# Optimization experiments

Hardware: AMD Instinct MI355X
Metric: run time of the kernel (lower is better)

## Reference

```python
import jax, jax.numpy as jnp
import numpy as np
from jax import lax

ORDER = 6
WN = 0.5 / 50.0          # highpass_cutoff / (orig_fs/2)
UP, DOWN = 16, 25        # 64/100 reduced by gcd 4 (scipy resample_poly)
HALF_LEN = 10 * DOWN     # scipy kaiser half length = 10*max_rate
NTAPS = 2 * HALF_LEN + 1
PADLEN = 21              # sosfiltfilt default: 3*(2*n_sections+1), 3 biquads
CHANNELS = np.array([126, 125, 48, 112, 67, 93, 10, 61, 39, 108])
D_MODEL = 16
LN_EPS = 1e-5


def _butter_hp_sos(order, wn):
    # scipy.signal.butter(order, wn, btype='high', output='sos') in pure numpy
    fs = 2.0
    warped = 2.0 * fs * np.tan(np.pi * wn / fs)
    m = np.arange(-order + 1, order, 2)
    p = -np.exp(1j * np.pi * m / (2 * order))     # analog LP prototype poles
    k = np.real(1.0 / np.prod(-p))                # lp2hp gain (no zeros)
    p = warped / p                                # lp2hp poles; zeros at s=0
    z = np.zeros(order)
    fs2 = 2.0 * fs                                # bilinear, fs=2
    k = k * np.real(np.prod(fs2 - z) / np.prod(fs2 - p))
    z = (fs2 + z) / (fs2 - z)                     # digital zeros, all +1
    p = (fs2 + p) / (fs2 - p)
    pp = p[np.imag(p) > 0]
    pp = pp[np.argsort(-np.abs(np.abs(pp) - 1.0))]  # closest to unit circle last
    sos = []
    for i, pi in enumerate(pp):
        b = np.array([1.0, -2.0, 1.0]) * (k if i == 0 else 1.0)
        a = np.array([1.0, -2.0 * pi.real, np.abs(pi) ** 2])
        sos.append(np.concatenate([b, a]))
    return np.array(sos)


def _sosfilt_zi(sos):
    # scipy.signal.sosfilt_zi: steady-state of step response per section
    n = sos.shape[0]
    zi = np.zeros((n, 2))
    scale = 1.0
    for s in range(n):
        b0, b1, b2, _, a1, a2 = sos[s]
        A = np.array([[1.0 + a1, -1.0], [a2, 1.0]])
        B = np.array([b1 - a1 * b0, b2 - a2 * b0])
        zi[s] = scale * np.linalg.solve(A, B)
        scale *= (b0 + b1 + b2) / (1.0 + a1 + a2)
    return zi


SOS = _butter_hp_sos(ORDER, WN)
ZI = _sosfilt_zi(SOS)


def _resample_fir():
    # scipy firwin(2*half_len+1, 1/max_rate, window=('kaiser',5.0)) * up
    fc = 1.0 / DOWN
    m = np.arange(NTAPS) - (NTAPS - 1) / 2.0
    h = fc * np.sinc(fc * m) * np.kaiser(NTAPS, 5.0)
    h /= h.sum()
    return h * UP


H_BASE = _resample_fir()


def _pos_encoding(max_len, d):
    pos = np.arange(max_len)[:, None].astype(np.float64)
    div = np.exp(np.arange(0, d, 2) * (-np.log(10000.0) / d))
    pe = np.zeros((max_len, d))
    pe[:, 0::2] = np.sin(pos * div)
    pe[:, 1::2] = np.cos(pos * div)
    return pe.astype(np.float32)


PE = _pos_encoding(3840, D_MODEL)


def _sosfilt(x, zi):
    # x: (N,T), zi: (N,3,2). Cascade of biquads, transposed direct form II.
    sos = jnp.asarray(SOS, x.dtype)
    nsec = SOS.shape[0]

    def step(z, xt):
        v = xt
        zs = []
        for s in range(nsec):  # fixed tiny cascade, unrolled inside scan
            b0, b1, b2, a1, a2 = sos[s, 0], sos[s, 1], sos[s, 2], sos[s, 4], sos[s, 5]
            y = b0 * v + z[s][0]
            zs.append((b1 * v - a1 * y + z[s][1], b2 * v - a2 * y))
            v = y
        return tuple(zs), v

    z0 = tuple((zi[:, s, 0], zi[:, s, 1]) for s in range(nsec))
    _, y = lax.scan(step, z0, x.T)
    return y.T


def _sosfiltfilt(x):
    # scipy.signal.sosfiltfilt with default odd padding, padlen=21
    zi = jnp.asarray(ZI, x.dtype)
    front = 2.0 * x[:, :1] - x[:, PADLEN:0:-1]
    back = 2.0 * x[:, -1:] - x[:, -2:-PADLEN - 2:-1]
    ext = jnp.concatenate([front, x, back], axis=1)
    y = _sosfilt(ext, zi[None] * ext[:, 0, None, None])
    y = y[:, ::-1]
    y = _sosfilt(y, zi[None] * y[:, 0, None, None])
    return y[:, ::-1][:, PADLEN:-PADLEN]


def _resample_poly(x):
    # scipy.signal.resample_poly(x, 64, 100): upfirdn via dilated conv
    T = x.shape[-1]
    n_out = (T * UP) // DOWN + int((T * UP) % DOWN != 0)
    n_pre_pad = DOWN - HALF_LEN % DOWN
    n_pre_remove = (HALF_LEN + n_pre_pad) // DOWN

    def outlen(lh):
        return (((T - 1) * UP + lh) - 1) // DOWN + 1

    n_post = 0
    while outlen(NTAPS + n_pre_pad + n_post) < n_out + n_pre_remove:
        n_post += 1
    h = np.concatenate([np.zeros(n_pre_pad), H_BASE, np.zeros(n_post)])
    L = h.size
    rhs = jnp.asarray(h[::-1].copy(), x.dtype).reshape(1, 1, L)
    y = lax.conv_general_dilated(x[:, None, :], rhs, window_strides=(DOWN,),
                                 padding=[(L - 1, L - 1)], lhs_dilation=(UP,),
                                 dimension_numbers=('NCH', 'OIH', 'NCH'))
    return y[:, 0, n_pre_remove:n_pre_remove + n_out]


def _ln(x, g, b):
    mu = x.mean(-1, keepdims=True)
    var = ((x - mu) ** 2).mean(-1, keepdims=True)
    return (x - mu) * lax.rsqrt(var + LN_EPS) * g + b


def setup_inputs() -> dict:
    key = jax.random.key(0)
    ks = jax.random.split(key, 20)
    f32 = jnp.float32
    d = {
        'x': jax.random.normal(ks[0], (64, 128, 2000), f32),
        'conv_w': jax.random.normal(ks[1], (16, 10, 3), f32) * 0.15,
        'conv_b': jnp.zeros((16,), f32),
        'ln0_g': jnp.ones((16,), f32), 'ln0_b': jnp.zeros((16,), f32),
        'wqkv': jax.random.normal(ks[2], (48, 16), f32) * 0.125,
        'bqkv': jnp.zeros((48,), f32),
        'wo': jax.random.normal(ks[3], (16, 16), f32) * 0.25,
        'bo': jnp.zeros((16,), f32),
        'w1': jax.random.normal(ks[4], (32, 16), f32) * 0.2,
        'b1': jnp.zeros((32,), f32),
        'w2': jax.random.normal(ks[5], (16, 32), f32) * 0.2,
        'b2': jnp.zeros((16,), f32),
        'ln1_g': jnp.ones((16,), f32), 'ln1_b': jnp.zeros((16,), f32),
        'ln2_g': jnp.ones((16,), f32), 'ln2_b': jnp.zeros((16,), f32),
        'wfc': jax.random.normal(ks[6], (1, 16), f32) * 0.3,
        'bfc': jnp.zeros((1,), f32),
    }
    return d


def reference(x, conv_w, conv_b, ln0_g, ln0_b, wqkv, bqkv, wo, bo,
              w1, b1, w2, b2, ln1_g, ln1_b, ln2_g, ln2_b, wfc, bfc):
    B = x.shape[0]
    # remove Cz (last channel) then gather interesting channels
    x = x[:, :-1, :][:, jnp.asarray(CHANNELS), :]        # (B,10,T)
    x = x - x.mean(axis=1, keepdims=True)                # CAR
    C, T = x.shape[1], x.shape[2]
    xf = _sosfiltfilt(x.reshape(B * C, T))               # zero-phase highpass
    xr = _resample_poly(xf)                              # 100 Hz -> 64 Hz
    x = xr.reshape(B, C, -1)
    x = jnp.tanh(x)                                      # artifact_scale = 1.0
    mean = x.mean(axis=2, keepdims=True)                 # zscore, unbiased std
    var = ((x - mean) ** 2).sum(axis=2, keepdims=True) / (x.shape[2] - 1)
    std = jnp.maximum(jnp.sqrt(var), 1e-6)
    x = (x - mean) / std
    # conv1d k=3 pad=1 (10 -> 16) + relu
    x = lax.conv_general_dilated(x, conv_w, (1,), [(1, 1)],
                                 dimension_numbers=('NCH', 'OIH', 'NCH'))
    x = jax.nn.relu(x + conv_b[None, :, None])
    x = x.transpose(0, 2, 1)                             # (B,S,16)
    x = _ln(x, ln0_g, ln0_b)
    x = x + jnp.asarray(PE[:x.shape[1]], x.dtype)[None]
    # TransformerEncoderLayer, post-norm, nhead=1, relu FFN (eval: no dropout)
    qkv = x @ wqkv.T + bqkv
    q, k, v = jnp.split(qkv, 3, axis=-1)
    att = jax.nn.softmax(jnp.einsum('bqd,bkd->bqk', q, k) * 0.25, axis=-1)
    a = jnp.einsum('bqk,bkd->bqd', att, v) @ wo.T + bo
    x = _ln(x + a, ln1_g, ln1_b)
    f = jax.nn.relu(x @ w1.T + b1) @ w2.T + b2
    x = _ln(x + f, ln2_g, ln2_b)
    pooled = x.mean(axis=1)                              # adaptive avg pool -> 1
    return pooled @ wfc.T + bfc                          # (B,1)
```

## Files before the change

### kernel.cpp

```cpp
#include <hip/hip_runtime.h>
#include <cmath>
#include <complex>
#include <algorithm>

#ifndef M_PI
#define M_PI 3.14159265358979323846
#endif

typedef _Float16 f16x8 __attribute__((ext_vector_type(8)));
typedef _Float16 f16x4 __attribute__((ext_vector_type(4)));
typedef float f32x4 __attribute__((ext_vector_type(4)));

struct FiltArg {
  double b0[3], b1[3], b2[3], a1[3], a2[3];
  double zi0[3], zi1[3];
};
struct CorArg { double CA[16 * 6]; };
struct EigArg {
  double Pm[36], Pinv[36];
  double czi[6];
  double lam_re[3], lam_im[3];
  double lami_re[3], lami_im[3];
};
struct FirArg { float h[526]; };

static void design_sos(FiltArg& sa) {
  const int order = 6;
  const double wn = 0.5 / 50.0;
  const double fs = 2.0;
  double warped = 2.0 * fs * std::tan(M_PI * wn / fs);
  std::complex<double> p[6];
  for (int i = 0; i < order; i++) {
    int m = -order + 1 + 2 * i;
    p[i] = -std::exp(std::complex<double>(0.0, M_PI * m / (2.0 * order)));
  }
  std::complex<double> prod1(1, 0);
  for (int i = 0; i < 6; i++) prod1 *= -p[i];
  double k = (1.0 / prod1).real();
  for (int i = 0; i < 6; i++) p[i] = warped / p[i];
  const double fs2 = 2.0 * fs;
  std::complex<double> num(1, 0), den(1, 0);
  for (int i = 0; i < 6; i++) { num *= fs2; den *= (fs2 - p[i]); }
  k *= (num / den).real();
  for (int i = 0; i < 6; i++) p[i] = (fs2 + p[i]) / (fs2 - p[i]);
  std::complex<double> pp[3]; int n = 0;
  for (int i = 0; i < 6; i++) if (p[i].imag() > 0) pp[n++] = p[i];
  std::stable_sort(pp, pp + 3,
    [](const std::complex<double>& A, const std::complex<double>& B) {
      return std::fabs(std::abs(A) - 1.0) > std::fabs(std::abs(B) - 1.0);
    });
  double sos[3][6];
  for (int s = 0; s < 3; s++) {
    double g = (s == 0) ? k : 1.0;
    sos[s][0] = g; sos[s][1] = -2.0 * g; sos[s][2] = g;
    sos[s][3] = 1.0; sos[s][4] = -2.0 * pp[s].real(); sos[s][5] = std::norm(pp[s]);
  }
  double scale = 1.0;
  for (int s = 0; s < 3; s++) {
    double b0 = sos[s][0], b1 = sos[s][1], b2 = sos[s][2];
    double a1 = sos[s][4], a2 = sos[s][5];
    double det = 1.0 + a1 + a2;
    double r0 = b1 - a1 * b0, r1 = b2 - a2 * b0;
    double z0 = (r0 + r1) / det;
    double z1 = ((1.0 + a1) * r1 - a2 * r0) / det;
    sa.b0[s] = b0; sa.b1[s] = b1; sa.b2[s] = b2; sa.a1[s] = a1; sa.a2[s] = a2;
    sa.zi0[s] = scale * z0; sa.zi1[s] = scale * z1;
    scale *= (b0 + b1 + b2) / (1.0 + a1 + a2);
  }
}

static double host_step(const FiltArg& c, double z[6], double v) {
  for (int s = 0; s < 3; s++) {
    double y = c.b0[s] * v + z[2 * s];
    z[2 * s]     = c.b1[s] * v - c.a1[s] * y + z[2 * s + 1];
    z[2 * s + 1] = c.b2[s] * v - c.a2[s] * y;
    v = y;
  }
  return v;
}

static void build_filt(FiltArg& c, CorArg& co) {
  design_sos(c);
  for (int j = 0; j < 6; j++) {
    double z[6] = {0, 0, 0, 0, 0, 0};
    z[j] = 1.0;
    for (int i = 0; i < 16; i++) co.CA[i * 6 + j] = host_step(c, z, 0.0);
  }
}

static void build_eig(const FiltArg& c, EigArg& e) {
  double Pr[36];
  for (int s = 0; s < 3; s++) {
    double a1 = c.a1[s], a2 = c.a2[s];
    std::complex<double> disc = std::sqrt(std::complex<double>(a1 * a1 - 4.0 * a2, 0.0));
    std::complex<double> p = (-a1 + disc) / 2.0;
    if (p.imag() < 0) p = std::conj(p);
    std::complex<double> v[6] = {0, 0, 0, 0, 0, 0};
    v[2 * s] = 1.0;
    v[2 * s + 1] = a1 + p;
    std::complex<double> y = 1.0;
    for (int j = s + 1; j < 3; j++) {
      double b0j = c.b0[j], b1j = c.b1[j], b2j = c.b2[j];
      double a1j = c.a1[j], a2j = c.a2[j];
      std::complex<double> det = p * p + a1j * p + a2j;
      std::complex<double> r0 = (b1j - a1j * b0j) * y;
      std::complex<double> r1 = (b2j - a2j * b0j) * y;
      std::complex<double> z0 = (p * r0 + r1) / det;
      std::complex<double> z1 = ((p + a1j) * r1 - a2j * r0) / det;
      v[2 * j] = z0; v[2 * j + 1] = z1;
      y = b0j * y + z0;
    }
    for (int i = 0; i < 6; i++) {
      Pr[i * 6 + 2 * s]     = v[i].real();
      Pr[i * 6 + 2 * s + 1] = v[i].imag();
    }
    std::complex<double> lam = std::pow(p, 16);
    e.lam_re[s] = lam.real(); e.lam_im[s] = lam.imag();
    std::complex<double> li = 1.0 / lam;
    e.lami_re[s] = li.real(); e.lami_im[s] = li.imag();
  }
  for (int i = 0; i < 36; i++) e.Pm[i] = Pr[i];
  double M[6][12];
  for (int i = 0; i < 6; i++)
    for (int j = 0; j < 6; j++) { M[i][j] = Pr[i * 6 + j]; M[i][6 + j] = (i == j) ? 1.0 : 0.0; }
  for (int col = 0; col < 6; col++) {
    int piv = col;
    for (int i = col + 1; i < 6; i++)
      if (std::fabs(M[i][col]) > std::fabs(M[piv][col])) piv = i;
    if (piv != col) for (int j = 0; j < 12; j++) std::swap(M[col][j], M[piv][j]);
    double d = M[col][col];
    for (int j = 0; j < 12; j++) M[col][j] /= d;
    for (int i = 0; i < 6; i++) if (i != col) {
      double f = M[i][col];
      for (int j = 0; j < 12; j++) M[i][j] -= f * M[col][j];
    }
  }
  for (int i = 0; i < 6; i++)
    for (int j = 0; j < 6; j++) e.Pinv[i * 6 + j] = M[i][6 + j];
  double zv[6];
  for (int s = 0; s < 3; s++) { zv[2 * s] = c.zi0[s]; zv[2 * s + 1] = c.zi1[s]; }
  for (int i = 0; i < 6; i++) {
    double sum = 0.0;
    for (int j = 0; j < 6; j++) sum += e.Pinv[i * 6 + j] * zv[j];
    e.czi[i] = sum;
  }
}

static double bessel_i0(double x) {
  double s = 1.0, t = 1.0;
  for (int k = 1; k < 64; k++) {
    double u = x / (2.0 * k);
    t *= u * u; s += t;
    if (t < 1e-18 * s) break;
  }
  return s;
}

static void design_fir(FirArg& fa) {
  double h[501];
  const double fc = 1.0 / 25.0;
  double denom = bessel_i0(5.0);
  double sum = 0.0;
  for (int nn = 0; nn < 501; nn++) {
    double m = nn - 250.0;
    double xx = fc * m;
    double snc = (nn == 250) ? 1.0 : std::sin(M_PI * xx) / (M_PI * xx);
    double r = (2.0 * nn) / 500.0 - 1.0;
    double w = bessel_i0(5.0 * std::sqrt(std::max(0.0, 1.0 - r * r))) / denom;
    h[nn] = fc * snc * w; sum += h[nn];
  }
  for (int nn = 0; nn < 25; nn++) fa.h[nn] = 0.0f;
  for (int nn = 0; nn < 501; nn++) fa.h[25 + nn] = (float)(h[nn] / sum * 16.0);
}

__device__ inline double waveReduceSum(double v) {
  #pragma unroll
  for (int off = 32; off > 0; off >>= 1) v += __shfl_down(v, off, 64);
  return v;
}

__device__ inline void cpow_int(double br, double bi, int n, double& rr_, double& ri_) {
  double rr = 1.0, ri = 0.0;
  while (n) {
    if (n & 1) { double t = rr * br - ri * bi; ri = rr * bi + ri * br; rr = t; }
    double t2 = br * br - bi * bi; bi = 2.0 * br * bi; br = t2;
    n >>= 1;
  }
  rr_ = rr; ri_ = ri;
}

__global__ __launch_bounds__(256) void k_chansel_pe(const float* __restrict__ x,
                                                    float* __restrict__ xs,
                                                    float* __restrict__ pe,
                                                    float* __restrict__ out) {
  int gid = blockIdx.x;
  if (gid < 500) {
    int idx = gid * 256 + threadIdx.x;
    int b = idx / 2000, t = idx % 2000;
    const int ch[10] = {126, 125, 48, 112, 67, 93, 10, 61, 39, 108};
    const float* xb = x + (size_t)b * 128 * 2000;
    float v[10]; float s = 0.f;
    #pragma unroll
    for (int c = 0; c < 10; c++) { v[c] = xb[ch[c] * 2000 + t]; s += v[c]; }
    s *= 0.1f;
    #pragma unroll
    for (int c = 0; c < 10; c++) xs[((size_t)b * 10 + c) * 2000 + t] = v[c] - s;
  } else {
    int i = (gid - 500) * 256 + threadIdx.x;
    int t = i >> 4, d = i & 15, j = d >> 1;
    double div = exp(-((double)(2 * j)) * 0.5756462732485114);
    double a = (double)t * div;
    pe[i] = (float)((d & 1) ? cos(a) : sin(a));
    if (gid == 579 && threadIdx.x < 64) out[threadIdx.x] = 0.f;
  }
}

#define XR(t) xr[(t) + ((t) >> 5)]
#define YF(t) yf[(t) + ((t) >> 5)]
__global__ __launch_bounds__(128) void k_filtfilt(float* __restrict__ xs,
                                                  FiltArg c, CorArg co, EigArg eg) {
  __shared__ float xr[2112];
  __shared__ double yf[2112];
  __shared__ double wsum[3][2];
  int r = blockIdx.x;
  int gk = threadIdx.x;
  int lane = gk & 63;
  int wv = gk >> 6;
  float* x = xs + (size_t)r * 2000;

  float x0f = x[0], xlf = x[1999];
  for (int t = gk; t < 2048; t += 128) {
    float v;
    if (t < 21)        v = 2.f * x0f - x[21 - t];
    else if (t < 2021) v = x[t - 21];
    else if (t < 2042) v = 2.f * xlf - x[4019 - t];
    else               v = 0.f;
    XR(t) = v;
  }
  __syncthreads();

  double b0[3], b1[3], b2[3], a1[3], a2[3];
  #pragma unroll
  for (int s = 0; s < 3; s++) {
    b0[s] = c.b0[s]; b1[s] = c.b1[s]; b2[s] = c.b2[s];
    a1[s] = c.a1[s]; a2[s] = c.a2[s];
  }
  auto step = [&](double* z, double v) -> double {
    #pragma unroll
    for (int s = 0; s < 3; s++) {
      double y = b0[s] * v + z[2 * s];
      z[2 * s]     = b1[s] * v - a1[s] * y + z[2 * s + 1];
      z[2 * s + 1] = b2[s] * v - a2[s] * y;
      v = y;
    }
    return v;
  };

  auto eigscan = [&](double seed, const double* F, double* zst) {
    double G[6];
    #pragma unroll
    for (int i = 0; i < 6; i++) {
      double s = 0.0;
      #pragma unroll
      for (int j = 0; j < 6; j++) s += eg.Pinv[i * 6 + j] * F[j];
      G[i] = s;
    }
    double tre[3], tim[3], sre[3], sim[3];
    #pragma unroll
    for (int s3 = 0; s3 < 3; s3++) {
      double gre = G[2 * s3], gim = -G[2 * s3 + 1];
      double mre, mim;
      cpow_int(eg.lami_re[s3], eg.lami_im[s3], gk, mre, mim);
      tre[s3] = mre * gre - mim * gim;
      tim[s3] = mre * gim + mim * gre;
      double pr = tre[s3], pi = tim[s3];
      #pragma unroll
      for (int off = 1; off < 64; off <<= 1) {
        double ore = __shfl_up(pr, off, 64);
        double oim = __shfl_up(pi, off, 64);
        pr += (lane >= off) ? ore : 0.0;
        pi += (lane >= off) ? oim : 0.0;
      }
      sre[s3] = pr; sim[s3] = pi;
      if (wv == 0 && lane == 63) { wsum[s3][0] = pr; wsum[s3][1] = pi; }
    }
    __syncthreads();
    double coord[6];
    #pragma unroll
    for (int s3 = 0; s3 < 3; s3++) {
      double inc_re = sre[s3] + (wv ? wsum[s3][0] : 0.0);
      double inc_im = sim[s3] + (wv ? wsum[s3][1] : 0.0);
      double Sre = inc_re - tre[s3], Sim = inc_im - tim[s3];
      double c0re = seed * eg.czi[2 * s3];
      double c0im = -seed * eg.czi[2 * s3 + 1];
      double lkre, lkim;
      cpow_int(eg.lam_re[s3], eg.lam_im[s3], gk, lkre, lkim);
      double lm1re = lkre * eg.lami_re[s3] - lkim * eg.lami_im[s3];
      double lm1im = lkre * eg.lami_im[s3] + lkim * eg.lami_re[s3];
      if (gk == 0) { lm1re = 0.0; lm1im = 0.0; }
      double cre = lkre * c0re - lkim * c0im + lm1re * Sre - lm1im * Sim;
      double cim = lkre * c0im + lkim * c0re + lm1re * Sim + lm1im * Sre;
      coord[2 * s3] = cre;
      coord[2 * s3 + 1] = -cim;
    }
    #pragma unroll
    for (int i = 0; i < 6; i++) {
      double s = 0.0;
      #pragma unroll
      for (int j = 0; j < 6; j++) s += eg.Pm[i * 6 + j] * coord[j];
      zst[i] = s;
    }
  };

  int t0 = gk * 16;
  double z[6], yreg[16], zst[6];

  #pragma unroll
  for (int i = 0; i < 6; i++) z[i] = 0.0;
  for (int i = 0; i < 16; i++) yreg[i] = step(z, (double)XR(t0 + i));
  eigscan((double)XR(0), z, zst);
  for (int i = 0; i < 16; i++) {
    double corr = 0.0;
    #pragma unroll
    for (int j = 0; j < 6; j++) corr += co.CA[i * 6 + j] * zst[j];
    YF(t0 + i) = yreg[i] + corr;
  }
  __syncthreads();

  auto rin = [&](int j) -> double { return (j <= 2041) ? YF(2041 - j) : 0.0; };
  double seedB = YF(2041);
  #pragma unroll
  for (int i = 0; i < 6; i++) z[i] = 0.0;
  for (int i = 0; i < 16; i++) yreg[i] = step(z, rin(t0 + i));
  eigscan(seedB, z, zst);
  for (int i = 0; i < 16; i++) {
    int j = t0 + i;
    if (j >= 21 && j <= 2020) {
      double corr = 0.0;
      #pragma unroll
      for (int jj = 0; jj < 6; jj++) corr += co.CA[i * 6 + jj] * zst[jj];
      x[2020 - j] = (float)(yreg[i] + corr);
    }
  }
}

__global__ __launch_bounds__(256) void k_resample_norm(const float* __restrict__ xf,
                                                       float* __restrict__ xn,
                                                       FirArg fa) {
  __shared__ float xl[2000];
  __shared__ float hl[526];
  int r = blockIdx.x;
  const float* x = xf + (size_t)r * 2000;
  for (int i = threadIdx.x; i < 2000; i += 256) xl[i] = x[i];
  for (int i = threadIdx.x; i < 526; i += 256) hl[i] = fa.h[i];
  __syncthreads();
  float vals[5];
  #pragma unroll
  for (int kk = 0; kk < 5; kk++) {
    int o = threadIdx.x + kk * 256;
    int P = 25 * (o + 11);
    int phase = P & 15;
    float acc = 0.f;
    for (int m = phase; m <= 525; m += 16) {
      int idx = (P - m) >> 4;
      if (idx >= 0 && idx < 2000) acc += hl[m] * xl[idx];
    }
    vals[kk] = tanhf(acc);
  }
  double s = 0.0, ss = 0.0;
  #pragma unroll
  for (int kk = 0; kk < 5; kk++) {
    s += (double)vals[kk]; ss += (double)vals[kk] * (double)vals[kk];
  }
  s = waveReduceSum(s); ss = waveReduceSum(ss);
  __shared__ double red[8];
  int wid = threadIdx.x >> 6, lane = threadIdx.x & 63;
  if (lane == 0) { red[wid] = s; red[4 + wid] = ss; }
  __syncthreads();
  double S = red[0] + red[1] + red[2] + red[3];
  double SS = red[4] + red[5] + red[6] + red[7];
  double mean = S / 1280.0;
  double var = (SS - 1280.0 * mean * mean) / 1279.0;
  double sd = fmax(sqrt(fmax(var, 0.0)), 1e-6);
  float fmean = (float)mean, finv = (float)(1.0 / sd);
  #pragma unroll
  for (int kk = 0; kk < 5; kk++)
    xn[(size_t)r * 1280 + threadIdx.x + kk * 256] = (vals[kk] - fmean) * finv;
}

__global__ __launch_bounds__(256) void k_conv_ln_pe_qkv(const float* __restrict__ xn,
    const float* __restrict__ cw, const float* __restrict__ cb,
    const float* __restrict__ g0, const float* __restrict__ bt0,
    const float* __restrict__ wqkv, const float* __restrict__ bqkv,
    const float* __restrict__ pe,
    float* __restrict__ x0, float* __restrict__ Q,
    _Float16* __restrict__ Kp, _Float16* __restrict__ Vt_g) {
  __shared__ float w[480], bias[16], gg[16], gb[16];
  __shared__ float wq[768], bq[48];
  for (int i = threadIdx.x; i < 480; i += 256) w[i] = cw[i];
  for (int i = threadIdx.x; i < 768; i += 256) wq[i] = wqkv[i];
  if (threadIdx.x < 16) {
    bias[threadIdx.x] = cb[threadIdx.x];
    gg[threadIdx.x] = g0[threadIdx.x];
    gb[threadIdx.x] = bt0[threadIdx.x];
  }
  if (threadIdx.x < 48) bq[threadIdx.x] = bqkv[threadIdx.x];
  __syncthreads();
  int idx = blockIdx.x * 256 + threadIdx.x;
  int b = idx / 1280, t = idx % 1280;
  const float* xb = xn + (size_t)b * 10 * 1280;
  float in[10][3];
  #pragma unroll
  for (int i = 0; i < 10; i++)
    #pragma unroll
    for (int k = 0; k < 3; k++) {
      int tt = t - 1 + k;
      in[i][k] = (tt >= 0 && tt < 1280) ? xb[i * 1280 + tt] : 0.f;
    }
  float o[16];
  #pragma unroll
  for (int oc = 0; oc < 16; oc++) {
    float a = bias[oc];
    #pragma unroll
    for (int i = 0; i < 10; i++)
      #pragma unroll
      for (int k = 0; k < 3; k++) a += in[i][k] * w[oc * 30 + i * 3 + k];
    o[oc] = fmaxf(a, 0.f);
  }
  float mu = 0.f;
  #pragma unroll
  for (int d = 0; d < 16; d++) mu += o[d];
  mu *= (1.f / 16.f);
  float var = 0.f;
  #pragma unroll
  for (int d = 0; d < 16; d++) { float dd = o[d] - mu; var += dd * dd; }
  var *= (1.f / 16.f);
  float inv = 1.f / sqrtf(var + 1e-5f);
  float xv[16];
  float* outp = x0 + (size_t)idx * 16;
  const float* pep = pe + t * 16;
  #pragma unroll
  for (int d = 0; d < 16; d++) {
    xv[d] = (o[d] - mu) * inv * gg[d] + gb[d] + pep[d];
    outp[d] = xv[d];
  }
  float* qp = Q + (size_t)idx * 16;
  #pragma unroll
  for (int j = 0; j < 16; j++) {
    float a = bq[j];
    #pragma unroll
    for (int d = 0; d < 16; d++) a += xv[d] * wq[j * 16 + d];
    qp[j] = a;
  }
  {
    _Float16* kp = Kp + (size_t)idx * 32;
    #pragma unroll
    for (int j = 0; j < 16; j++) {
      float a = bq[16 + j];
      #pragma unroll
      for (int d = 0; d < 16; d++) a += xv[d] * wq[(16 + j) * 16 + d];
      kp[j] = (_Float16)a;
    }
    f16x8 zz;
    #pragma unroll
    for (int j = 0; j < 8; j++) zz[j] = (_Float16)0.f;
    *(f16x8*)&kp[16] = zz;
    *(f16x8*)&kp[24] = zz;
  }
  {
    _Float16* vt = Vt_g + (size_t)b * 16 * 1280 + t;
    #pragma unroll
    for (int j = 0; j < 16; j++) {
      float a = bq[32 + j];
      #pragma unroll
      for (int d = 0; d < 16; d++) a += xv[d] * wq[(32 + j) * 16 + d];
      vt[j * 1280] = (_Float16)a;
    }
  }
}

#define ATT_SHIFT 12.0f
__global__ __launch_bounds__(256) void k_attn_mfma(const float* __restrict__ Q,
    const _Float16* __restrict__ Kp, const _Float16* __restrict__ Vt_g,
    float* __restrict__ A) {
  __shared__ __align__(16) _Float16 Ks2[64 * 32];
  __shared__ __align__(16) _Float16 Vt[16 * 72];
  __shared__ __align__(16) _Float16 Pld[4][16 * 40];
  int tid = threadIdx.x;
  int b  = blockIdx.x / 20;
  int rg = blockIdx.x % 20;
  int wv = tid >> 6;
  int lane = tid & 63;
  int col = lane & 15;
  int quad = lane >> 4;
  size_t base = (size_t)b * 1280;
  int row0 = rg * 64 + wv * 16;

  f16x8 qf;
  #pragma unroll
  for (int j = 0; j < 8; j++) qf[j] = (_Float16)0.f;
  if (quad < 2) {
    const float* qp = Q + (base + row0 + col) * 16 + quad * 8;
    #pragma unroll
    for (int j = 0; j < 8; j++) qf[j] = (_Float16)(0.25f * qp[j]);
  }
  f32x4 oacc = {0.f, 0.f, 0.f, 0.f};
  float lacc = 0.f;

  const _Float16* vt_b = Vt_g + (size_t)b * 16 * 1280;

  for (int s = 0; s < 20; s++) {
    __syncthreads();
    *(f16x8*)&Ks2[tid * 8] =
        *(const f16x8*)(Kp + (base + s * 64) * 32 + tid * 8);
    if (tid < 128) {
      int d = tid >> 3, qc = tid & 7;
      *(f16x8*)&Vt[d * 72 + qc * 8] =
          *(const f16x8*)(vt_b + d * 1280 + s * 64 + qc * 8);
    }
    __syncthreads();
    #pragma unroll
    for (int c = 0; c < 2; c++) {
      #pragma unroll
      for (int t = 0; t < 2; t++) {
        int keyoff = c * 32 + t * 16;
        f16x8 af = *(f16x8*)&Ks2[(keyoff + col) * 32 + quad * 8];
        f32x4 sf = {0.f, 0.f, 0.f, 0.f};
        sf = __builtin_amdgcn_mfma_f32_16x16x32_f16(af, qf, sf, 0, 0, 0);
        f16x4 ph;
        float psum = 0.f;
        #pragma unroll
        for (int r = 0; r < 4; r++) {
          float p = __expf(sf[r] - ATT_SHIFT);
          psum += p;
          ph[r] = (_Float16)p;
        }
        lacc += psum;
        *(f16x4*)&Pld[wv][col * 40 + t * 16 + quad * 4] = ph;
      }
      __syncthreads();
      f16x8 pf = *(f16x8*)&Pld[wv][col * 40 + quad * 8];
      f16x8 vf = *(f16x8*)&Vt[col * 72 + c * 32 + quad * 8];
      oacc = __builtin_amdgcn_mfma_f32_16x16x32_f16(pf, vf, oacc, 0, 0, 0);
      __syncthreads();
    }
  }
  lacc += __shfl_xor(lacc, 16, 64);
  lacc += __shfl_xor(lacc, 32, 64);
  #pragma unroll
  for (int r = 0; r < 4; r++) {
    float lr = __shfl(lacc, quad * 4 + r, 64);
    A[(base + row0 + quad * 4 + r) * 16 + col] = oacc[r] / lr;
  }
}

__global__ __launch_bounds__(256) void k_combine_pool(
    const float* __restrict__ A, const float* __restrict__ x0,
    const float* __restrict__ wo, const float* __restrict__ bo,
    const float* __restrict__ w1, const float* __restrict__ b1,
    const float* __restrict__ w2, const float* __restrict__ b2,
    const float* __restrict__ g1, const float* __restrict__ bb1,
    const float* __restrict__ g2, const float* __restrict__ bb2,
    const float* __restrict__ wfc, const float* __restrict__ bfc,
    float* __restrict__ out) {
  __shared__ float swo[256], sw1[512], sw2[512];
  __shared__ float sbo[16], sb1[32], sb2[16], sg1[16], sbb1[16], sg2[16], sbb2[16];
  __shared__ float swf[16];
  int tid = threadIdx.x;
  swo[tid] = wo[tid];
  for (int i = tid; i < 512; i += 256) { sw1[i] = w1[i]; sw2[i] = w2[i]; }
  if (tid < 16) {
    sbo[tid] = bo[tid]; sb2[tid] = b2[tid];
    sg1[tid] = g1[tid]; sbb1[tid] = bb1[tid];
    sg2[tid] = g2[tid]; sbb2[tid] = bb2[tid];
    swf[tid] = wfc[tid];
  }
  if (tid < 32) sb1[tid] = b1[tid];
  __syncthreads();

  int idx = blockIdx.x * 256 + tid;
  int bb = blockIdx.x / 5;
  const float* pa = A + (size_t)idx * 16;
  float a[16];
  #pragma unroll
  for (int d = 0; d < 16; d++) a[d] = pa[d];
  float h[16];
  const float* xr = x0 + (size_t)idx * 16;
  #pragma unroll
  for (int d = 0; d < 16; d++) {
    float o = sbo[d];
    #pragma unroll
    for (int e = 0; e < 16; e++) o += a[e] * swo[d * 16 + e];
    h[d] = xr[d] + o;
  }
  float mu = 0.f;
  #pragma unroll
  for (int d = 0; d < 16; d++) mu += h[d];
  mu *= (1.f / 16.f);
  float var = 0.f;
  #pragma unroll
  for (int d = 0; d < 16; d++) { float dd = h[d] - mu; var += dd * dd; }
  var *= (1.f / 16.f);
  float inv = 1.f / sqrtf(var + 1e-5f);
  float x1[16];
  #pragma unroll
  for (int d = 0; d < 16; d++) x1[d] = (h[d] - mu) * inv * sg1[d] + sbb1[d];
  float t1[32];
  #pragma unroll
  for (int j = 0; j < 32; j++) {
    float u = sb1[j];
    #pragma unroll
    for (int d = 0; d < 16; d++) u += x1[d] * sw1[j * 16 + d];
    t1[j] = fmaxf(u, 0.f);
  }
  float h2[16];
  #pragma unroll
  for (int d = 0; d < 16; d++) {
    float u = sb2[d];
    #pragma unroll
    for (int j = 0; j < 32; j++) u += t1[j] * sw2[d * 32 + j];
    h2[d] = x1[d] + u;
  }
  mu = 0.f;
  #pragma unroll
  for (int d = 0; d < 16; d++) mu += h2[d];
  mu *= (1.f / 16.f);
  var = 0.f;
  #pragma unroll
  for (int d = 0; d < 16; d++) { float dd = h2[d] - mu; var += dd * dd; }
  var *= (1.f / 16.f);
  inv = 1.f / sqrtf(var + 1e-5f);
  float pv = 0.f;
  #pragma unroll
  for (int d = 0; d < 16; d++)
    pv += ((h2[d] - mu) * inv * sg2[d] + sbb2[d]) * swf[d];
  double part = waveReduceSum((double)pv);
  __shared__ double red[4];
  int wid = tid >> 6, lane = tid & 63;
  if (lane == 0) red[wid] = part;
  __syncthreads();
  if (tid == 0) {
    double S = red[0] + red[1] + red[2] + red[3];
    float add = (float)(S / 1280.0);
    if (blockIdx.x % 5 == 0) add += bfc[0];
    atomicAdd(&out[bb], add);
  }
}

extern "C" void kernel_launch(void* const* d_in, const int* in_sizes, int n_in,
                              void* d_out, int out_size, void* d_ws, size_t ws_size,
                              hipStream_t stream) {
  const float* x    = (const float*)d_in[0];
  const float* cw   = (const float*)d_in[1];
  const float* cb   = (const float*)d_in[2];
  const float* g0   = (const float*)d_in[3];
  const float* bt0  = (const float*)d_in[4];
  const float* wqkv = (const float*)d_in[5];
  const float* bqkv = (const float*)d_in[6];
  const float* wo   = (const float*)d_in[7];
  const float* bo   = (const float*)d_in[8];
  const float* w1   = (const float*)d_in[9];
  const float* b1   = (const float*)d_in[10];
  const float* w2   = (const float*)d_in[11];
  const float* b2   = (const float*)d_in[12];
  const float* g1   = (const float*)d_in[13];
  const float* bb1  = (const float*)d_in[14];
  const float* g2   = (const float*)d_in[15];
  const float* bb2  = (const float*)d_in[16];
  const float* wfc  = (const float*)d_in[17];
  const float* bfc  = (const float*)d_in[18];
  float* out = (float*)d_out;

  float* ws = (float*)d_ws;
  float* xs = ws;
  float* y1 = xs + 1280000;
  float* xn = y1 + 1306880;
  float* x0 = xn + 819200;
  float* Q  = x0 + 1310720;
  _Float16* Kp   = (_Float16*)(Q + 1310720);
  _Float16* Vt_g = (_Float16*)(Q + 2621440);
  float* pe = Q + 2621440 + 655360;
  float* Abuf = ws;

  FiltArg fc; CorArg co; EigArg eg; FirArg fa;
  build_filt(fc, co);
  build_eig(fc, eg);
  design_fir(fa);

  k_chansel_pe<<<580, 256, 0, stream>>>(x, xs, pe, out);
  k_filtfilt<<<640, 128, 0, stream>>>(xs, fc, co, eg);
  k_resample_norm<<<640, 256, 0, stream>>>(xs, xn, fa);
  k_conv_ln_pe_qkv<<<320, 256, 0, stream>>>(xn, cw, cb, g0, bt0, wqkv, bqkv,
                                            pe, x0, Q, Kp, Vt_g);
  k_attn_mfma<<<1280, 256, 0, stream>>>(Q, Kp, Vt_g, Abuf);
  k_combine_pool<<<320, 256, 0, stream>>>(Abuf, x0, wo, bo, w1, b1, w2, b2,
                                          g1, bb1, g2, bb2, wfc, bfc, out);
}
```

Measured before the change: 235.5 us.

## Fuse attention output projection, FFN and pooling into attention kernel

Merges the post-attention combine and pool stage into the MFMA attention kernel. The normalized attention outputs are staged in shared memory and one wavefront per block runs the output projection, both layer norms, the FFN and the pooled reduction. This removes the global round trip for the attention buffer and one kernel launch. In exchange, the tail work runs on only 64 of 256 threads per block, adds shared memory and register pressure, and quadruples the number of atomic adds to the output.

After: 229.3 us (median of 2 runs). -2.6%, faster.

```diff
diff --git a/kernel.cpp b/kernel.cpp
--- a/kernel.cpp
+++ b/kernel.cpp
@@ -480,12 +480,23 @@
 }
 
 #define ATT_SHIFT 12.0f
-__global__ __launch_bounds__(256) void k_attn_mfma(const float* __restrict__ Q,
+__global__ __launch_bounds__(256) void k_attn_combine(const float* __restrict__ Q,
     const _Float16* __restrict__ Kp, const _Float16* __restrict__ Vt_g,
-    float* __restrict__ A) {
+    const float* __restrict__ x0,
+    const float* __restrict__ wo, const float* __restrict__ bo,
+    const float* __restrict__ w1, const float* __restrict__ b1,
+    const float* __restrict__ w2, const float* __restrict__ b2,
+    const float* __restrict__ g1, const float* __restrict__ bb1,
+    const float* __restrict__ g2, const float* __restrict__ bb2,
+    const float* __restrict__ wfc, const float* __restrict__ bfc,
+    float* __restrict__ out) {
   __shared__ __align__(16) _Float16 Ks2[64 * 32];
   __shared__ __align__(16) _Float16 Vt[16 * 72];
   __shared__ __align__(16) _Float16 Pld[4][16 * 40];
+  __shared__ float Aly[64][17];
+  __shared__ float swo[256], sw1[512], sw2[512];
+  __shared__ float sbo[16], sb1[32], sb2[16], sg1[16], sbb1[16], sg2[16], sbb2[16];
+  __shared__ float swf[16];
   int tid = threadIdx.x;
   int b  = blockIdx.x / 20;
   int rg = blockIdx.x % 20;
@@ -495,6 +506,16 @@
   int quad = lane >> 4;
   size_t base = (size_t)b * 1280;
   int row0 = rg * 64 + wv * 16;
+
+  swo[tid] = wo[tid];
+  for (int i = tid; i < 512; i += 256) { sw1[i] = w1[i]; sw2[i] = w2[i]; }
+  if (tid < 16) {
+    sbo[tid] = bo[tid]; sb2[tid] = b2[tid];
+    sg1[tid] = g1[tid]; sbb1[tid] = bb1[tid];
+    sg2[tid] = g2[tid]; sbb2[tid] = bb2[tid];
+    swf[tid] = wfc[tid];
+  }
+  if (tid < 32) sb1[tid] = b1[tid];
 
   f16x8 qf;
   #pragma unroll
@@ -550,100 +571,72 @@
   #pragma unroll
   for (int r = 0; r < 4; r++) {
     float lr = __shfl(lacc, quad * 4 + r, 64);
-    A[(base + row0 + quad * 4 + r) * 16 + col] = oacc[r] / lr;
-  }
-}
-
-__global__ __launch_bounds__(256) void k_combine_pool(
-    const float* __restrict__ A, const float* __restrict__ x0,
-    const float* __restrict__ wo, const float* __restrict__ bo,
-    const float* __restrict__ w1, const float* __restrict__ b1,
-    const float* __restrict__ w2, const float* __restrict__ b2,
-    const float* __restrict__ g1, const float* __restrict__ bb1,
-    const float* __restrict__ g2, const float* __restrict__ bb2,
-    const float* __restrict__ wfc, const float* __restrict__ bfc,
-    float* __restrict__ out) {
-  __shared__ float swo[256], sw1[512], sw2[512];
-  __shared__ float sbo[16], sb1[32], sb2[16], sg1[16], sbb1[16], sg2[16], sbb2[16];
-  __shared__ float swf[16];
-  int tid = threadIdx.x;
-  swo[tid] = wo[tid];
-  for (int i = tid; i < 512; i += 256) { sw1[i] = w1[i]; sw2[i] = w2[i]; }
-  if (tid < 16) {
-    sbo[tid] = bo[tid]; sb2[tid] = b2[tid];
-    sg1[tid] = g1[tid]; sbb1[tid] = bb1[tid];
-    sg2[tid] = g2[tid]; sbb2[tid] = bb2[tid];
-    swf[tid] = wfc[tid];
-  }
-  if (tid < 32) sb1[tid] = b1[tid];
+    Aly[wv * 16 + quad * 4 + r][col] = oacc[r] / lr;
+  }
   __syncthreads();
 
-  int idx = blockIdx.x * 256 + tid;
-  int bb = blockIdx.x / 5;
-  const float* pa = A + (size_t)idx * 16;
-  float a[16];
-  #pragma unroll
-  for (int d = 0; d < 16; d++) a[d] = pa[d];
-  float h[16];
-  const float* xr = x0 + (size_t)idx * 16;
-  #pragma unroll
-  for (int d = 0; d < 16; d++) {
-    float o = sbo[d];
-    #pragma unroll
-    for (int e = 0; e < 16; e++) o += a[e] * swo[d * 16 + e];
-    h[d] = xr[d] + o;
-  }
-  float mu = 0.f;
-  #pragma unroll
-  for (int d = 0; d < 16; d++) mu += h[d];
-  mu *= (1.f / 16.f);
-  float var = 0.f;
-  #pragma unroll
-  for (int d = 0; d < 16; d++) { float dd = h[d] - mu; var += dd * dd; }
-  var *= (1.f / 16.f);
-  float inv = 1.f / sqrtf(var + 1e-5f);
-  float x1[16];
-  #pragma unroll
-  for (int d = 0; d < 16; d++) x1[d] = (h[d] - mu) * inv * sg1[d] + sbb1[d];
-  float t1[32];
-  #pragma unroll
-  for (int j = 0; j < 32; j++) {
-    float u = sb1[j];
-    #pragma unroll
-    for (int d = 0; d < 16; d++) u += x1[d] * sw1[j * 16 + d];
-    t1[j] = fmaxf(u, 0.f);
-  }
-  float h2[16];
-  #pragma unroll
-  for (int d = 0; d < 16; d++) {
-    float u = sb2[d];
-    #pragma unroll
-    for (int j = 0; j < 32; j++) u += t1[j] * sw2[d * 32 + j];
-    h2[d] = x1[d] + u;
-  }
-  mu = 0.f;
-  #pragma unroll
-  for (int d = 0; d < 16; d++) mu += h2[d];
-  mu *= (1.f / 16.f);
-  var = 0.f;
-  #pragma unroll
-  for (int d = 0; d < 16; d++) { float dd = h2[d] - mu; var += dd * dd; }
-  var *= (1.f / 16.f);
-  inv = 1.f / sqrtf(var + 1e-5f);
-  float pv = 0.f;
-  #pragma unroll
-  for (int d = 0; d < 16; d++)
-    pv += ((h2[d] - mu) * inv * sg2[d] + sbb2[d]) * swf[d];
-  double part = waveReduceSum((double)pv);
-  __shared__ double red[4];
-  int wid = tid >> 6, lane = tid & 63;
-  if (lane == 0) red[wid] = part;
-  __syncthreads();
-  if (tid == 0) {
-    double S = red[0] + red[1] + red[2] + red[3];
-    float add = (float)(S / 1280.0);
-    if (blockIdx.x % 5 == 0) add += bfc[0];
-    atomicAdd(&out[bb], add);
+  if (tid < 64) {
+    int grow = rg * 64 + tid;
+    size_t goff = (base + grow) * 16;
+    float a[16];
+    #pragma unroll
+    for (int d = 0; d < 16; d++) a[d] = Aly[tid][d];
+    float h[16];
+    const float* xr = x0 + goff;
+    #pragma unroll
+    for (int d = 0; d < 16; d++) {
+      float o = sbo[d];
+      #pragma unroll
+      for (int e = 0; e < 16; e++) o += a[e] * swo[d * 16 + e];
+      h[d] = xr[d] + o;
+    }
+    float mu = 0.f;
+    #pragma unroll
+    for (int d = 0; d < 16; d++) mu += h[d];
+    mu *= (1.f / 16.f);
+    float var = 0.f;
+    #pragma unroll
+    for (int d = 0; d < 16; d++) { float dd = h[d] - mu; var += dd * dd; }
+    var *= (1.f / 16.f);
+    float inv = 1.f / sqrtf(var + 1e-5f);
+    float x1[16];
+    #pragma unroll
+    for (int d = 0; d < 16; d++) x1[d] = (h[d] - mu) * inv * sg1[d] + sbb1[d];
+    float t1[32];
+    #pragma unroll
+    for (int j = 0; j < 32; j++) {
+      float u = sb1[j];
+      #pragma unroll
+      for (int d = 0; d < 16; d++) u += x1[d] * sw1[j * 16 + d];
+      t1[j] = fmaxf(u, 0.f);
+    }
+    float h2[16];
+    #pragma unroll
+    for (int d = 0; d < 16; d++) {
+      float u = sb2[d];
+      #pragma unroll
+      for (int j = 0; j < 32; j++) u += t1[j] * sw2[d * 32 + j];
+      h2[d] = x1[d] + u;
+    }
+    mu = 0.f;
+    #pragma unroll
+    for (int d = 0; d < 16; d++) mu += h2[d];
+    mu *= (1.f / 16.f);
+    var = 0.f;
+    #pragma unroll
+    for (int d = 0; d < 16; d++) { float dd = h2[d] - mu; var += dd * dd; }
+    var *= (1.f / 16.f);
+    inv = 1.f / sqrtf(var + 1e-5f);
+    float pv = 0.f;
+    #pragma unroll
+    for (int d = 0; d < 16; d++)
+      pv += ((h2[d] - mu) * inv * sg2[d] + sbb2[d]) * swf[d];
+    double part = waveReduceSum((double)pv);
+    if (tid == 0) {
+      float add = (float)(part / 1280.0);
+      if (blockIdx.x % 20 == 0) add += bfc[0];
+      atomicAdd(&out[b], add);
+    }
   }
 }
 
@@ -680,7 +673,6 @@
   _Float16* Kp   = (_Float16*)(Q + 1310720);
   _Float16* Vt_g = (_Float16*)(Q + 2621440);
   float* pe = Q + 2621440 + 655360;
-  float* Abuf = ws;
 
   FiltArg fc; CorArg co; EigArg eg; FirArg fa;
   build_filt(fc, co);
@@ -692,7 +684,7 @@
   k_resample_norm<<<640, 256, 0, stream>>>(xs, xn, fa);
   k_conv_ln_pe_qkv<<<320, 256, 0, stream>>>(xn, cw, cb, g0, bt0, wqkv, bqkv,
                                             pe, x0, Q, Kp, Vt_g);
-  k_attn_mfma<<<1280, 256, 0, stream>>>(Q, Kp, Vt_g, Abuf);
-  k_combine_pool<<<320, 256, 0, stream>>>(Abuf, x0, wo, bo, w1, b1, w2, b2,
-                                          g1, bb1, g2, bb2, wfc, bfc, out);
-}
+  k_attn_combine<<<1280, 256, 0, stream>>>(Q, Kp, Vt_g, x0, wo, bo, w1, b1,
+                                           w2, b2, g1, bb1, g2, bb2, wfc, bfc,
+                                           out);
+}
```
